# Kernel tuning notes

Hardware: AMD Instinct MI355X
Metric: run time of the kernel (lower is better)

Reference implementation:

```python
import jax, jax.numpy as jnp
import numpy as np

D_MODEL = 1024
NUM_HEADS = 16
HEAD_DIM = D_MODEL // NUM_HEADS  # 64
THETA = 10000.0
BATCH = 4
SEQ = 2048


def _rope(v, pos):
    # v: (n, h, s, d) with d even; pairs are interleaved: (..., d//2, 2)
    n, h, s, d = v.shape
    j = jnp.arange(d // 2, dtype=v.dtype)
    inv_freq = THETA ** (-2.0 * j / d)                     # (d/2,)
    angles = pos.astype(v.dtype)[:, None] * inv_freq[None, :]  # (s, d/2)
    c = jnp.cos(angles)[None, None]                        # (1,1,s,d/2)
    sn = jnp.sin(angles)[None, None]
    vb = v.reshape(n, h, s, d // 2, 2)
    x0, x1 = vb[..., 0], vb[..., 1]
    y0 = x0 * c - x1 * sn
    y1 = x0 * sn + x1 * c
    return jnp.stack([y0, y1], axis=-1).reshape(n, h, s, d)


def setup_inputs() -> dict:
    key = jax.random.key(0)
    ks = jax.random.split(key, 5)
    x = jax.random.normal(ks[0], (BATCH, SEQ, D_MODEL), dtype=jnp.float32)
    token_positions = jnp.arange(SEQ, dtype=jnp.int32)
    scale = 0.02  # keep activations in a numerically sane range
    W_Q = jax.random.normal(ks[1], (D_MODEL, D_MODEL), dtype=jnp.float32) * scale
    W_K = jax.random.normal(ks[2], (D_MODEL, D_MODEL), dtype=jnp.float32) * scale
    W_V = jax.random.normal(ks[3], (D_MODEL, D_MODEL), dtype=jnp.float32) * scale
    W_O = jax.random.normal(ks[4], (D_MODEL, D_MODEL), dtype=jnp.float32) * scale
    return {"x": x, "token_positions": token_positions,
            "W_Q": W_Q, "W_K": W_K, "W_V": W_V, "W_O": W_O}


def reference(x, token_positions, W_Q, W_K, W_V, W_O):
    n, s, _ = x.shape
    h, d = NUM_HEADS, HEAD_DIM
    # projections: Linear stores W as (out, in), applies x @ W.T
    Q = (x @ W_Q.T).reshape(n, s, h, d).transpose(0, 2, 1, 3)  # (n,h,s,d)
    K = (x @ W_K.T).reshape(n, s, h, d).transpose(0, 2, 1, 3)
    V = (x @ W_V.T).reshape(n, s, h, d).transpose(0, 2, 1, 3)
    Q = _rope(Q, token_positions)
    K = _rope(K, token_positions)
    scores = jnp.einsum('nhqd,nhkd->nhqk', Q, K) * (d ** -0.5)
    causal = jnp.tril(jnp.ones((s, s), dtype=bool))
    scores = jnp.where(causal[None, None], scores, -jnp.inf)
    attn = jax.nn.softmax(scores, axis=-1)
    out = jnp.einsum('nhqk,nhkd->nhqd', attn, V)
    out = out.transpose(0, 2, 1, 3).reshape(n, s, h * d)
    return out @ W_O.T
```

## Files before the change

kernel.cpp:

```cpp
#include <hip/hip_runtime.h>
#include <math.h>

#define DM 1024
#define NH 16
#define HD 64
#define SQ 2048
#define NB 4
#define MR (NB*SQ)

typedef unsigned short ushort_t;
typedef __attribute__((ext_vector_type(8)))  short bf16x8;
typedef __attribute__((ext_vector_type(4)))  float f32x4;
typedef __attribute__((ext_vector_type(16))) float f32x16;

__device__ __forceinline__ ushort_t f2bf(float f) {
    unsigned u = __float_as_uint(f);
    return (ushort_t)((u + 0x7fffu + ((u >> 16) & 1u)) >> 16);
}
__device__ __forceinline__ float bf2f(ushort_t u) {
    return __uint_as_float((unsigned)u << 16);
}

__device__ __forceinline__ void gload16(const void* g, void* l) {
    __builtin_amdgcn_global_load_lds(
        (const __attribute__((address_space(1))) void*)g,
        (__attribute__((address_space(3))) void*)l, 16, 0, 0);
}

__device__ __forceinline__ unsigned cvtpk_bf16(float a, float b) {
    unsigned r;
    asm volatile("v_cvt_pk_bf16_f32 %0, %1, %2" : "=v"(r) : "v"(a), "v"(b));
    return r;
}

__global__ __launch_bounds__(256)
void f2bf_kernel(const float* __restrict__ in, ushort_t* __restrict__ out) {
    int i = (blockIdx.x * 256 + threadIdx.x) * 4;
    float4 v = *reinterpret_cast<const float4*>(&in[i]);
    ushort4 o;
    o.x = f2bf(v.x); o.y = f2bf(v.y); o.z = f2bf(v.z); o.w = f2bf(v.w);
    *reinterpret_cast<ushort4*>(&out[i]) = o;
}

__global__ __launch_bounds__(256)
void w4_convert(const float* __restrict__ w0, const float* __restrict__ w1,
                const float* __restrict__ w2, const float* __restrict__ w3,
                ushort_t* __restrict__ out) {
    int i = (blockIdx.x * 256 + threadIdx.x) * 4;
    const int WSZ = DM * DM;
    const float* src = (i < WSZ) ? w0 : (i < 2 * WSZ) ? w1
                     : (i < 3 * WSZ) ? w2 : w3;
    int off = i & (WSZ - 1);
    float4 v = *reinterpret_cast<const float4*>(&src[off]);
    ushort4 o;
    o.x = f2bf(v.x); o.y = f2bf(v.y); o.z = f2bf(v.z); o.w = f2bf(v.w);
    *reinterpret_cast<ushort4*>(&out[i]) = o;
}

template<int MODE>
__global__ __launch_bounds__(256)
void gemm_bf16_bt(const ushort_t* __restrict__ A, const ushort_t* __restrict__ B,
                  void* __restrict__ Cv, int M, int N, int K, float scale)
{
    __shared__ ushort_t As[128 * 32];
    __shared__ ushort_t Bs[128 * 32];

    const int tid = threadIdx.x;
    const int w  = tid >> 6;
    const int l  = tid & 63;
    const int wr = w >> 1, wc = w & 1;
    const int arow0 = blockIdx.y * 128;
    const int bcol0 = blockIdx.x * 128;
    const int lr = l & 15;
    const int kg = l >> 4;

    const int srow[2] = { (w * 2 + 0) * 16 + (l >> 2), (w * 2 + 1) * 16 + (l >> 2) };
    const int scol = (l & 3) * 8;

    f32x4 acc[4][4] = {};

    for (int k0 = 0; k0 < K; k0 += 32) {
        #pragma unroll
        for (int q = 0; q < 2; ++q) {
            int chunk = w * 2 + q;
            gload16(&A[(size_t)(arow0 + srow[q]) * K + k0 + scol], &As[chunk * 512]);
            gload16(&B[(size_t)(bcol0 + srow[q]) * K + k0 + scol], &Bs[chunk * 512]);
        }
        __syncthreads();

        bf16x8 af[4], bfr[4];
        #pragma unroll
        for (int m = 0; m < 4; ++m)
            af[m] = *reinterpret_cast<const bf16x8*>(
                        &As[(wr * 64 + m * 16 + lr) * 32 + kg * 8]);
        #pragma unroll
        for (int nn = 0; nn < 4; ++nn)
            bfr[nn] = *reinterpret_cast<const bf16x8*>(
                        &Bs[(wc * 64 + nn * 16 + lr) * 32 + kg * 8]);

        #pragma unroll
        for (int m = 0; m < 4; ++m)
            #pragma unroll
            for (int nn = 0; nn < 4; ++nn)
                acc[m][nn] = __builtin_amdgcn_mfma_f32_16x16x32_bf16(
                    af[m], bfr[nn], acc[m][nn], 0, 0, 0);
        __syncthreads();
    }

    const int crow = kg * 4;
    #pragma unroll
    for (int m = 0; m < 4; ++m) {
        #pragma unroll
        for (int nn = 0; nn < 4; ++nn) {
            #pragma unroll
            for (int r = 0; r < 4; ++r) {
                int row = arow0 + wr * 64 + m * 16 + crow + r;
                int col = bcol0 + wc * 64 + nn * 16 + lr;
                float v = acc[m][nn][r] * scale;
                if (MODE == 0) {
                    ((float*)Cv)[(size_t)row * N + col] = v;
                } else if (MODE == 1) {
                    int nb = row >> 11, s = row & (SQ - 1);
                    int hh = col >> 6,  d = col & 63;
                    ((ushort_t*)Cv)[(((size_t)nb * NH + hh) * SQ + s) * HD + d] = f2bf(v);
                } else {
                    int hh = row >> 6,  d = row & 63;
                    int nb = col >> 11, s = col & (SQ - 1);
                    ((ushort_t*)Cv)[(((size_t)nb * NH + hh) * HD + d) * SQ + s] = f2bf(v);
                }
            }
        }
    }
}

__global__ __launch_bounds__(256)
void rope_bf16(ushort_t* __restrict__ Q, ushort_t* __restrict__ K,
               const int* __restrict__ pos)
{
    int t = blockIdx.x * 256 + threadIdx.x;
    int j  = t & 31;
    int s  = (t >> 5) & (SQ - 1);
    int nh = t >> 16;
    size_t base = ((size_t)nh * SQ + s) * HD + 2 * j;

    float p = (float)pos[s];
    float inv = exp2f(-0.41524101186072848f * (float)j);
    float sn, cs;
    sincosf(p * inv, &sn, &cs);

    ushort2 q2 = *reinterpret_cast<ushort2*>(&Q[base]);
    ushort2 k2 = *reinterpret_cast<ushort2*>(&K[base]);
    float qx = bf2f(q2.x), qy = bf2f(q2.y);
    float kx = bf2f(k2.x), ky = bf2f(k2.y);
    ushort2 qo, ko;
    qo.x = f2bf(qx * cs - qy * sn);  qo.y = f2bf(qx * sn + qy * cs);
    ko.x = f2bf(kx * cs - ky * sn);  ko.y = f2bf(kx * sn + ky * cs);
    *reinterpret_cast<ushort2*>(&Q[base]) = qo;
    *reinterpret_cast<ushort2*>(&K[base]) = ko;
}

__global__ __launch_bounds__(256)
void flash_mfma(const ushort_t* __restrict__ Q, const ushort_t* __restrict__ K,
                const ushort_t* __restrict__ Vt, ushort_t* __restrict__ O)
{
    __shared__ ushort_t Ks [64 * 64];
    __shared__ ushort_t Vts[64 * 64];

    const int tid  = threadIdx.x;
    const int wq   = tid >> 6;
    const int lane = tid & 63;
    const int q5   = lane & 31;
    const int g    = lane >> 5;
    const int qb   = blockIdx.x;
    const int h    = blockIdx.y;
    const int n    = blockIdx.z;

    const size_t hb = (size_t)(n * NH + h);
    const ushort_t* Kp  = K  + hb * SQ * HD;
    const ushort_t* Vtp = Vt + hb * HD * SQ;

    const int qglob = qb * 128 + wq * 32 + q5;
    const int qwave = qb * 128 + wq * 32;
    const int qmaxw = qwave + 31;
    const int nt    = 2 * qb + 2;

    bf16x8 qf[4];
    {
        const ushort_t* Qr = Q + (hb * SQ + (size_t)qglob) * HD;
        #pragma unroll
        for (int s4 = 0; s4 < 4; ++s4)
            qf[s4] = *reinterpret_cast<const bf16x8*>(&Qr[s4 * 16 + g * 8]);
    }

    const int srowl = (lane >> 3);
    const int scole = ((lane & 7) ^ srowl) * 8;

    f32x16 o0 = {}, o1 = {};
    float m_run = -1e30f, l_run = 0.f;

    for (int t = 0; t < nt; ++t) {
        const int kvbase = t * 64;

        __syncthreads();
        #pragma unroll
        for (int qi = 0; qi < 2; ++qi) {
            int c = wq * 2 + qi;
            int row = c * 8 + srowl;
            gload16(&Kp [(size_t)(kvbase + row) * HD + scole], &Ks [c * 512]);
            gload16(&Vtp[(size_t)row * SQ + kvbase + scole],   &Vts[c * 512]);
        }
        __syncthreads();

        if (kvbase <= qmaxw) {
            f32x16 st0 = {}, st1 = {};
            #pragma unroll
            for (int s4 = 0; s4 < 4; ++s4) {
                {   int row = q5;
                    int c16 = (s4 * 2 + g) ^ (row & 7);
                    bf16x8 kf = *reinterpret_cast<const bf16x8*>(&Ks[row * 64 + c16 * 8]);
                    st0 = __builtin_amdgcn_mfma_f32_32x32x16_bf16(kf, qf[s4], st0, 0, 0, 0);
                }
                {   int row = 32 + q5;
                    int c16 = (s4 * 2 + g) ^ (row & 7);
                    bf16x8 kf = *reinterpret_cast<const bf16x8*>(&Ks[row * 64 + c16 * 8]);
                    st1 = __builtin_amdgcn_mfma_f32_32x32x16_bf16(kf, qf[s4], st1, 0, 0, 0);
                }
            }

            if (kvbase + 63 > qwave) {
                #pragma unroll
                for (int r = 0; r < 16; ++r) {
                    int kvr = kvbase + (r & 3) + 8 * (r >> 2) + 4 * g;
                    if (kvr      > qglob) st0[r] = -1e30f;
                    if (kvr + 32 > qglob) st1[r] = -1e30f;
                }
            }

            float pmax = -1e30f;
            #pragma unroll
            for (int r = 0; r < 16; ++r) {
                pmax = fmaxf(pmax, st0[r]);
                pmax = fmaxf(pmax, st1[r]);
            }
            pmax = fmaxf(pmax, __shfl_xor(pmax, 32));
            float mnew = fmaxf(m_run, pmax);

            float rs = 0.f;
            #pragma unroll
            for (int r = 0; r < 16; ++r) {
                st0[r] = __expf(st0[r] - mnew); rs += st0[r];
                st1[r] = __expf(st1[r] - mnew); rs += st1[r];
            }
            rs += __shfl_xor(rs, 32);

            float sc = __expf(m_run - mnew);
            l_run = l_run * sc + rs;
            m_run = mnew;

            #pragma unroll
            for (int r = 0; r < 16; ++r) {
                float scb = __shfl(sc, (r & 3) + 8 * (r >> 2) + 4 * g, 64);
                o0[r] *= scb;
                o1[r] *= scb;
            }

            #pragma unroll
            for (int s = 0; s < 4; ++s) {
                const int bA = (s & 1) * 8;
                const int bB = bA + 4;
                float pa0, pa1, pa2, pa3, pb0, pb1, pb2, pb3;
                if (s < 2) {
                    pa0 = st0[bA]; pa1 = st0[bA+1]; pa2 = st0[bA+2]; pa3 = st0[bA+3];
                    pb0 = st0[bB]; pb1 = st0[bB+1]; pb2 = st0[bB+2]; pb3 = st0[bB+3];
                } else {
                    pa0 = st1[bA]; pa1 = st1[bA+1]; pa2 = st1[bA+2]; pa3 = st1[bA+3];
                    pb0 = st1[bB]; pb1 = st1[bB+1]; pb2 = st1[bB+2]; pb3 = st1[bB+3];
                }
                unsigned wA0 = cvtpk_bf16(pa0, pa1), wA1 = cvtpk_bf16(pa2, pa3);
                unsigned wB0 = cvtpk_bf16(pb0, pb1), wB1 = cvtpk_bf16(pb2, pb3);

                unsigned send0 = g ? wA0 : wB0;
                unsigned send1 = g ? wA1 : wB1;
                unsigned recv0 = (unsigned)__shfl_xor((int)send0, 32, 64);
                unsigned recv1 = (unsigned)__shfl_xor((int)send1, 32, 64);

                unsigned d0 = g ? recv0 : wA0;
                unsigned d1 = g ? recv1 : wA1;
                unsigned d2 = g ? wB0 : recv0;
                unsigned d3 = g ? wB1 : recv1;

                int4 pi = make_int4((int)d0, (int)d1, (int)d2, (int)d3);
                bf16x8 pa = *reinterpret_cast<bf16x8*>(&pi);

                {   int row = q5;
                    int c16 = (s * 2 + g) ^ (row & 7);
                    bf16x8 vf = *reinterpret_cast<const bf16x8*>(&Vts[row * 64 + c16 * 8]);
                    o0 = __builtin_amdgcn_mfma_f32_32x32x16_bf16(pa, vf, o0, 0, 0, 0);
                }
                {   int row = 32 + q5;
                    int c16 = (s * 2 + g) ^ (row & 7);
                    bf16x8 vf = *reinterpret_cast<const bf16x8*>(&Vts[row * 64 + c16 * 8]);
                    o1 = __builtin_amdgcn_mfma_f32_32x32x16_bf16(pa, vf, o1, 0, 0, 0);
                }
            }
        }
    }

    float linv = 1.0f / l_run;
    #pragma unroll
    for (int r = 0; r < 16; ++r) {
        int qr = (r & 3) + 8 * (r >> 2) + 4 * g;
        float lb = __shfl(linv, qr, 64);
        size_t rowb = ((size_t)n * SQ + qb * 128 + wq * 32 + qr) * DM + h * 64;
        O[rowb + q5]      = f2bf(o0[r] * lb);
        O[rowb + 32 + q5] = f2bf(o1[r] * lb);
    }
}

extern "C" void kernel_launch(void* const* d_in, const int* in_sizes, int n_in,
                              void* d_out, int out_size, void* d_ws, size_t ws_size,
                              hipStream_t stream)
{
    const float* x   = (const float*)d_in[0];
    const int*   pos = (const int*)  d_in[1];
    const float* W_Q = (const float*)d_in[2];
    const float* W_K = (const float*)d_in[3];
    const float* W_V = (const float*)d_in[4];
    const float* W_O = (const float*)d_in[5];
    float* out = (float*)d_out;

    const size_t T   = (size_t)NB * SQ * DM;
    const size_t WSZ = (size_t)DM * DM;

    ushort_t* xb  = (ushort_t*)d_ws;
    ushort_t* Wb  = xb + T;
    ushort_t* Qb  = Wb + 4 * WSZ;
    ushort_t* Kb  = Qb + T;
    ushort_t* Vtb = Kb + T;
    ushort_t* Op  = xb;

    const ushort_t* WQb = Wb;
    const ushort_t* WKb = Wb + WSZ;
    const ushort_t* WVb = Wb + 2 * WSZ;
    const ushort_t* WOb = Wb + 3 * WSZ;

    f2bf_kernel<<<T / 1024, 256, 0, stream>>>(x, xb);
    w4_convert<<<4 * WSZ / 1024, 256, 0, stream>>>(W_Q, W_K, W_V, W_O, Wb);

    dim3 gQK(DM / 128, MR / 128);
    gemm_bf16_bt<1><<<gQK, 256, 0, stream>>>(xb, WQb, Qb, MR, DM, DM, 0.125f);
    gemm_bf16_bt<1><<<gQK, 256, 0, stream>>>(xb, WKb, Kb, MR, DM, DM, 1.0f);
    dim3 gV(MR / 128, DM / 128);
    gemm_bf16_bt<2><<<gV, 256, 0, stream>>>(WVb, xb, Vtb, DM, MR, DM, 1.0f);

    rope_bf16<<<(NB * NH * SQ * 32) / 256, 256, 0, stream>>>(Qb, Kb, pos);

    dim3 agrid(SQ / 128, NH, NB);
    flash_mfma<<<agrid, 256, 0, stream>>>(Qb, Kb, Vtb, Op);

    dim3 gO(DM / 128, MR / 128);
    gemm_bf16_bt<0><<<gO, 256, 0, stream>>>(Op, WOb, out, MR, DM, DM, 1.0f);
}
```

Measured before the change: 377.1 us.

## Fuse Q/K projections, double-buffer flash KV tiles, lazy softmax rescale

The Q and K projection GEMMs become one GEMM with N=2048 over the concatenated W_Q/W_K weights, and the epilogue routes columns to the Q or K buffer, scaling Q by 0.125. The flash attention kernel double-buffers its K/V LDS tiles so the next tile loads while the current one is computed, and it launches query blocks in reverse order so the longest causal blocks start first. The online softmax skips rescaling the accumulators unless the running max grows by more than 8, which removes shuffles and multiplies but allows exp values up to e^8 before normalisation. Double buffering doubles LDS use, which may reduce occupancy.

```diff
diff --git a/kernel.cpp b/kernel.cpp
--- a/kernel.cpp
+++ b/kernel.cpp
@@ -7,6 +7,7 @@
 #define SQ 2048
 #define NB 4
 #define MR (NB*SQ)
+#define TTOT ((size_t)MR * DM)
 
 typedef unsigned short ushort_t;
 typedef __attribute__((ext_vector_type(8)))  short bf16x8;
@@ -119,14 +120,18 @@
                 float v = acc[m][nn][r] * scale;
                 if (MODE == 0) {
                     ((float*)Cv)[(size_t)row * N + col] = v;
-                } else if (MODE == 1) {
-                    int nb = row >> 11, s = row & (SQ - 1);
-                    int hh = col >> 6,  d = col & 63;
-                    ((ushort_t*)Cv)[(((size_t)nb * NH + hh) * SQ + s) * HD + d] = f2bf(v);
-                } else {
+                } else if (MODE == 2) {
                     int hh = row >> 6,  d = row & 63;
                     int nb = col >> 11, s = col & (SQ - 1);
                     ((ushort_t*)Cv)[(((size_t)nb * NH + hh) * HD + d) * SQ + s] = f2bf(v);
+                } else {
+                    int nb = row >> 11, s = row & (SQ - 1);
+                    bool isq = (col < 1024);
+                    int cc = col & 1023;
+                    int hh = cc >> 6, d = cc & 63;
+                    size_t idx = (((size_t)nb * NH + hh) * SQ + s) * HD + d;
+                    float vv = isq ? v * 0.125f : v;
+                    ((ushort_t*)Cv)[(isq ? (size_t)0 : TTOT) + idx] = f2bf(vv);
                 }
             }
         }
@@ -163,15 +168,15 @@
 void flash_mfma(const ushort_t* __restrict__ Q, const ushort_t* __restrict__ K,
                 const ushort_t* __restrict__ Vt, ushort_t* __restrict__ O)
 {
-    __shared__ ushort_t Ks [64 * 64];
-    __shared__ ushort_t Vts[64 * 64];
+    __shared__ ushort_t Ks [2][64 * 64];
+    __shared__ ushort_t Vts[2][64 * 64];
 
     const int tid  = threadIdx.x;
     const int wq   = tid >> 6;
     const int lane = tid & 63;
     const int q5   = lane & 31;
     const int g    = lane >> 5;
-    const int qb   = blockIdx.x;
+    const int qb   = (gridDim.x - 1) - blockIdx.x;
     const int h    = blockIdx.y;
     const int n    = blockIdx.z;
 
@@ -195,21 +200,28 @@
     const int srowl = (lane >> 3);
     const int scole = ((lane & 7) ^ srowl) * 8;
 
-    f32x16 o0 = {}, o1 = {};
-    float m_run = -1e30f, l_run = 0.f;
-
-    for (int t = 0; t < nt; ++t) {
-        const int kvbase = t * 64;
-
-        __syncthreads();
+    auto stage = [&](int buf, int t) {
+        const int kvb = t * 64;
         #pragma unroll
         for (int qi = 0; qi < 2; ++qi) {
             int c = wq * 2 + qi;
             int row = c * 8 + srowl;
-            gload16(&Kp [(size_t)(kvbase + row) * HD + scole], &Ks [c * 512]);
-            gload16(&Vtp[(size_t)row * SQ + kvbase + scole],   &Vts[c * 512]);
+            gload16(&Kp [(size_t)(kvb + row) * HD + scole], &Ks [buf][c * 512]);
+            gload16(&Vtp[(size_t)row * SQ + kvb + scole],   &Vts[buf][c * 512]);
         }
-        __syncthreads();
+    };
+
+    f32x16 o0 = {}, o1 = {};
+    float m_run = -1e30f, l_run = 0.f;
+
+    stage(0, 0);
+    __syncthreads();
+
+    for (int t = 0; t < nt; ++t) {
+        const int cur = t & 1;
+        const int kvbase = t * 64;
+
+        if (t + 1 < nt) stage(cur ^ 1, t + 1);
 
         if (kvbase <= qmaxw) {
             f32x16 st0 = {}, st1 = {};
@@ -217,12 +229,12 @@
             for (int s4 = 0; s4 < 4; ++s4) {
                 {   int row = q5;
                     int c16 = (s4 * 2 + g) ^ (row & 7);
-                    bf16x8 kf = *reinterpret_cast<const bf16x8*>(&Ks[row * 64 + c16 * 8]);
+                    bf16x8 kf = *reinterpret_cast<const bf16x8*>(&Ks[cur][row * 64 + c16 * 8]);
                     st0 = __builtin_amdgcn_mfma_f32_32x32x16_bf16(kf, qf[s4], st0, 0, 0, 0);
                 }
                 {   int row = 32 + q5;
                     int c16 = (s4 * 2 + g) ^ (row & 7);
-                    bf16x8 kf = *reinterpret_cast<const bf16x8*>(&Ks[row * 64 + c16 * 8]);
+                    bf16x8 kf = *reinterpret_cast<const bf16x8*>(&Ks[cur][row * 64 + c16 * 8]);
                     st1 = __builtin_amdgcn_mfma_f32_32x32x16_bf16(kf, qf[s4], st1, 0, 0, 0);
                 }
             }
@@ -243,26 +255,28 @@
                 pmax = fmaxf(pmax, st1[r]);
             }
             pmax = fmaxf(pmax, __shfl_xor(pmax, 32));
-            float mnew = fmaxf(m_run, pmax);
+
+            if (!__all(pmax - m_run <= 8.0f)) {
+                float mnew = fmaxf(m_run, pmax);
+                float sc = __expf(m_run - mnew);
+                l_run *= sc;
+                #pragma unroll
+                for (int r = 0; r < 16; ++r) {
+                    float scb = __shfl(sc, (r & 3) + 8 * (r >> 2) + 4 * g, 64);
+                    o0[r] *= scb;
+                    o1[r] *= scb;
+                }
+                m_run = mnew;
+            }
 
             float rs = 0.f;
             #pragma unroll
             for (int r = 0; r < 16; ++r) {
-                st0[r] = __expf(st0[r] - mnew); rs += st0[r];
-                st1[r] = __expf(st1[r] - mnew); rs += st1[r];
+                st0[r] = __expf(st0[r] - m_run); rs += st0[r];
+                st1[r] = __expf(st1[r] - m_run); rs += st1[r];
             }
             rs += __shfl_xor(rs, 32);
-
-            float sc = __expf(m_run - mnew);
-            l_run = l_run * sc + rs;
-            m_run = mnew;
-
-            #pragma unroll
-            for (int r = 0; r < 16; ++r) {
-                float scb = __shfl(sc, (r & 3) + 8 * (r >> 2) + 4 * g, 64);
-                o0[r] *= scb;
-                o1[r] *= scb;
-            }
+            l_run += rs;
 
             #pragma unroll
             for (int s = 0; s < 4; ++s) {
@@ -294,16 +308,18 @@
 
                 {   int row = q5;
                     int c16 = (s * 2 + g) ^ (row & 7);
-                    bf16x8 vf = *reinterpret_cast<const bf16x8*>(&Vts[row * 64 + c16 * 8]);
+                    bf16x8 vf = *reinterpret_cast<const bf16x8*>(&Vts[cur][row * 64 + c16 * 8]);
                     o0 = __builtin_amdgcn_mfma_f32_32x32x16_bf16(pa, vf, o0, 0, 0, 0);
                 }
                 {   int row = 32 + q5;
                     int c16 = (s * 2 + g) ^ (row & 7);
-                    bf16x8 vf = *reinterpret_cast<const bf16x8*>(&Vts[row * 64 + c16 * 8]);
+                    bf16x8 vf = *reinterpret_cast<const bf16x8*>(&Vts[cur][row * 64 + c16 * 8]);
                     o1 = __builtin_amdgcn_mfma_f32_32x32x16_bf16(pa, vf, o1, 0, 0, 0);
                 }
             }
         }
+
+        __syncthreads();
     }
 
     float linv = 1.0f / l_run;
@@ -329,7 +345,7 @@
     const float* W_O = (const float*)d_in[5];
     float* out = (float*)d_out;
 
-    const size_t T   = (size_t)NB * SQ * DM;
+    const size_t T   = TTOT;
     const size_t WSZ = (size_t)DM * DM;
 
     ushort_t* xb  = (ushort_t*)d_ws;
@@ -339,17 +355,14 @@
     ushort_t* Vtb = Kb + T;
     ushort_t* Op  = xb;
 
-    const ushort_t* WQb = Wb;
-    const ushort_t* WKb = Wb + WSZ;
     const ushort_t* WVb = Wb + 2 * WSZ;
     const ushort_t* WOb = Wb + 3 * WSZ;
 
     f2bf_kernel<<<T / 1024, 256, 0, stream>>>(x, xb);
     w4_convert<<<4 * WSZ / 1024, 256, 0, stream>>>(W_Q, W_K, W_V, W_O, Wb);
 
-    dim3 gQK(DM / 128, MR / 128);
-    gemm_bf16_bt<1><<<gQK, 256, 0, stream>>>(xb, WQb, Qb, MR, DM, DM, 0.125f);
-    gemm_bf16_bt<1><<<gQK, 256, 0, stream>>>(xb, WKb, Kb, MR, DM, DM, 1.0f);
+    dim3 gQK(2048 / 128, MR / 128);
+    gemm_bf16_bt<3><<<gQK, 256, 0, stream>>>(xb, Wb, Qb, MR, 2048, DM, 1.0f);
     dim3 gV(MR / 128, DM / 128);
     gemm_bf16_bt<2><<<gV, 256, 0, stream>>>(WVb, xb, Vtb, DM, MR, DM, 1.0f);
 
```

Measured after the change: 354.4 us. -6.0%, faster.
